# Performance work log

Measured on AMD Instinct MI355X. Metric: run time of the kernel, lower is better.

Reference implementation:

```python
import jax, jax.numpy as jnp
import numpy as np

B, CH, T, D = 16, 64, 2048, 1  # d must be 1 (tf.squeeze(x, axis=-1))
F = 8  # conv filters


def setup_inputs() -> dict:
    key = jax.random.key(0)
    k1, k2, k3, k4 = jax.random.split(key, 4)
    return {
        "x": jax.random.normal(k1, (B, CH, T, D), dtype=jnp.float32),
        "w1": jax.random.normal(k2, (D, F), dtype=jnp.float32) * 0.1,
        "b1": jnp.zeros((F,), dtype=jnp.float32),
        "w2": jax.random.normal(k3, (D, F), dtype=jnp.float32) * 0.1,
        "b2": jnp.zeros((F,), dtype=jnp.float32),
        "gamma": jax.random.normal(k4, (1,), dtype=jnp.float32) * 0.1,
    }


def reference(x, w1, b1, w2, b2, gamma):
    b, ch, t, d = x.shape
    # 1x1 Conv2D == per-position matmul over channel dim; then Permute((2,1,3)) + Reshape((t,-1))
    q = (jnp.matmul(x, w1) + b1)  # (b, ch, t, F)
    k = (jnp.matmul(x, w2) + b2)  # (b, ch, t, F)
    q = jnp.transpose(q, (0, 2, 1, 3)).reshape(b, t, ch * q.shape[-1])  # (b, t, ch*F)
    k = jnp.transpose(k, (0, 2, 1, 3)).reshape(b, t, ch * k.shape[-1])  # (b, t, ch*F)
    energy = jnp.einsum('btf,bsf->bts', q, k)  # (b, t, t)
    max_h = jnp.max(energy, axis=2, keepdims=True)
    min_h = jnp.min(energy, axis=2, keepdims=True)
    energy = (energy - min_h) / (max_h - min_h + 1e-8)
    attention = jax.nn.softmax(energy, axis=-1)  # (b, t, t)
    x_sq = x[..., 0]  # (b, ch, t)
    # matmul(x_sq, attention, transpose_b=True): out[b,c,i] = sum_j x_sq[b,c,j] * attention[b,i,j]
    mixed = jnp.einsum('bcj,bij->bci', x_sq, attention)  # (b, ch, t)
    return gamma[0] * mixed[..., None] + x  # (b, ch, t, 1)
```

## Files before the change

kernel.cpp:

```cpp
#include <hip/hip_runtime.h>
#include <hip/hip_bf16.h>

#define NB 16
#define NCH 64
#define NT 2048

typedef __attribute__((ext_vector_type(8)))  short bf8;
typedef __attribute__((ext_vector_type(4)))  short bf4;
typedef __attribute__((ext_vector_type(16))) float f16f;

#if defined(__has_builtin)
#if __has_builtin(__builtin_amdgcn_exp2f)
#define EXP2(x) __builtin_amdgcn_exp2f(x)
#else
#define EXP2(x) __expf((x) * 0.69314718056f)
#endif
#else
#define EXP2(x) __expf((x) * 0.69314718056f)
#endif

static __device__ __forceinline__ short f2b(float f) {
    unsigned u = __float_as_uint(f);
    u += 0x7fffu + ((u >> 16) & 1u);
    return (short)(u >> 16);
}

static __device__ __forceinline__ unsigned cvtpk(float lo, float hi) {
    unsigned r;
    asm("v_cvt_pk_bf16_f32 %0, %1, %2" : "=v"(r) : "v"(lo), "v"(hi));
    return r;
}
#define SWAP32(x, y) asm volatile("v_permlane32_swap_b32 %0, %1" : "+v"(x), "+v"(y))

__global__ __launch_bounds__(256)
void prep_k(const float* __restrict__ x, const float* __restrict__ b1p,
            const float* __restrict__ w2,
            float* __restrict__ Xw, short* __restrict__ xT, short* __restrict__ xn) {
    __shared__ float T[NCH][65];
    const int b = blockIdx.y, t0 = blockIdx.x * 64;
    const int tid = threadIdx.x;
    const float* xb = x + (size_t)b * NCH * NT;

    const int tt = (tid & 15) * 4;
    #pragma unroll
    for (int co = 0; co < 4; ++co) {
        int c = co * 16 + (tid >> 4);
        float4 v = *reinterpret_cast<const float4*>(&xb[(size_t)c * NT + t0 + tt]);
        T[c][tt] = v.x; T[c][tt + 1] = v.y; T[c][tt + 2] = v.z; T[c][tt + 3] = v.w;
        bf4 w; w[0] = f2b(v.x); w[1] = f2b(v.y); w[2] = f2b(v.z); w[3] = f2b(v.w);
        *reinterpret_cast<bf4*>(&xn[((size_t)b * NCH + c) * NT + t0 + tt]) = w;
    }
    __syncthreads();
    if (tid < 64) {
        float s2b1 = 0.f;
        #pragma unroll
        for (int f = 0; f < 8; ++f) s2b1 += b1p[f] * w2[f];
        float s = 0.f;
        #pragma unroll
        for (int c = 0; c < NCH; ++c) s += T[c][tid];
        Xw[b * NT + t0 + tid] = s2b1 * s;
    }
    const int row = tid >> 2, cs = (tid & 3) * 16;
    bf8 v0, v1;
    #pragma unroll
    for (int u = 0; u < 8; ++u) v0[u] = f2b(T[cs + u][row]);
    #pragma unroll
    for (int u = 0; u < 8; ++u) v1[u] = f2b(T[cs + 8 + u][row]);
    short* dst = xT + ((size_t)b * NT + t0 + row) * NCH + cs;
    *reinterpret_cast<bf8*>(dst) = v0;
    *reinterpret_cast<bf8*>(dst + 8) = v1;
}

__global__ __launch_bounds__(256)
void attn9_k(const float* __restrict__ w1, const float* __restrict__ w2,
             const float* __restrict__ gp,
             const float* __restrict__ Xw, const short* __restrict__ xT,
             const short* __restrict__ xn, const float* __restrict__ x,
             float* __restrict__ out) {
    __shared__ float mMn[4][32];
    __shared__ float mMx[4][32];
    __shared__ float mPS[4][32];
    __shared__ float mAcc[4][32][66];

    const int b  = blockIdx.y;
    const int i0 = blockIdx.x * 32;
    const int tid  = threadIdx.x;
    const int h    = tid >> 6;
    const int lane = tid & 63;
    const int il   = lane & 31;
    const int hi   = lane >> 5;
    const int hi8  = hi * 8;

    float s11 = 0.f;
    #pragma unroll
    for (int f = 0; f < 8; ++f) s11 += w1[f] * w2[f];
    const float g = gp[0];

    const short* xTb = xT + (size_t)b * NT * NCH;
    const short* xnb = xn + (size_t)b * NCH * NT;
    const float* xb  = x + (size_t)b * NCH * NT;
    const float* Xwb = Xw + b * NT;

    const short* brow = xTb + (size_t)(i0 + il) * NCH + hi8;
    const bf8 Bg0 = *reinterpret_cast<const bf8*>(brow);
    const bf8 Bg1 = *reinterpret_cast<const bf8*>(brow + 16);
    const bf8 Bg2 = *reinterpret_cast<const bf8*>(brow + 32);
    const bf8 Bg3 = *reinterpret_cast<const bf8*>(brow + 48);

    float rmn = 3.0e38f, rmx = -3.0e38f;

    for (int t = 0; t < 16; ++t) {
        const int jt = h * 512 + t * 32;
        const short* arow = xTb + (size_t)(jt + il) * NCH + hi8;
        bf8 a0 = *reinterpret_cast<const bf8*>(arow);
        bf8 a1 = *reinterpret_cast<const bf8*>(arow + 16);
        bf8 a2 = *reinterpret_cast<const bf8*>(arow + 32);
        bf8 a3 = *reinterpret_cast<const bf8*>(arow + 48);
        f16f acc = {0.f};
        acc = __builtin_amdgcn_mfma_f32_32x32x16_bf16(a0, Bg0, acc, 0, 0, 0);
        acc = __builtin_amdgcn_mfma_f32_32x32x16_bf16(a1, Bg1, acc, 0, 0, 0);
        acc = __builtin_amdgcn_mfma_f32_32x32x16_bf16(a2, Bg2, acc, 0, 0, 0);
        acc = __builtin_amdgcn_mfma_f32_32x32x16_bf16(a3, Bg3, acc, 0, 0, 0);
        const float4 tw0 = *reinterpret_cast<const float4*>(Xwb + jt + 4 * hi);
        const float4 tw1 = *reinterpret_cast<const float4*>(Xwb + jt + 8 + 4 * hi);
        const float4 tw2 = *reinterpret_cast<const float4*>(Xwb + jt + 16 + 4 * hi);
        const float4 tw3 = *reinterpret_cast<const float4*>(Xwb + jt + 24 + 4 * hi);
        const float tw[16] = { tw0.x, tw0.y, tw0.z, tw0.w, tw1.x, tw1.y, tw1.z, tw1.w,
                               tw2.x, tw2.y, tw2.z, tw2.w, tw3.x, tw3.y, tw3.z, tw3.w };
        #pragma unroll
        for (int r = 0; r < 16; ++r) {
            float e = fmaf(s11, acc[r], tw[r]);
            rmn = fminf(rmn, e);
            rmx = fmaxf(rmx, e);
        }
    }
    rmn = fminf(rmn, __shfl_xor(rmn, 32, 64));
    rmx = fmaxf(rmx, __shfl_xor(rmx, 32, 64));
    if (lane < 32) { mMn[h][lane] = rmn; mMx[h][lane] = rmx; }
    __syncthreads();

    float mn = mMn[0][il], mx = mMx[0][il];
    #pragma unroll
    for (int w = 1; w < 4; ++w) {
        mn = fminf(mn, mMn[w][il]);
        mx = fmaxf(mx, mMx[w][il]);
    }
    const float inv2 = 1.44269504f / (mx - mn + 1e-8f);
    const float A  = s11 * inv2;
    const float KI = -mn * inv2;

    f16f macc0 = {0.f}, macc1 = {0.f};
    float ps = 0.f;

    for (int t = 0; t < 16; ++t) {
        const int jt = h * 512 + t * 32;
        const short* arow = xTb + (size_t)(jt + il) * NCH + hi8;
        bf8 a0 = *reinterpret_cast<const bf8*>(arow);
        bf8 a1 = *reinterpret_cast<const bf8*>(arow + 16);
        bf8 a2 = *reinterpret_cast<const bf8*>(arow + 32);
        bf8 a3 = *reinterpret_cast<const bf8*>(arow + 48);
        f16f acc = {0.f};
        acc = __builtin_amdgcn_mfma_f32_32x32x16_bf16(a0, Bg0, acc, 0, 0, 0);
        acc = __builtin_amdgcn_mfma_f32_32x32x16_bf16(a1, Bg1, acc, 0, 0, 0);
        acc = __builtin_amdgcn_mfma_f32_32x32x16_bf16(a2, Bg2, acc, 0, 0, 0);
        acc = __builtin_amdgcn_mfma_f32_32x32x16_bf16(a3, Bg3, acc, 0, 0, 0);
        const float4 tw0 = *reinterpret_cast<const float4*>(Xwb + jt + 4 * hi);
        const float4 tw1 = *reinterpret_cast<const float4*>(Xwb + jt + 8 + 4 * hi);
        const float4 tw2 = *reinterpret_cast<const float4*>(Xwb + jt + 16 + 4 * hi);
        const float4 tw3 = *reinterpret_cast<const float4*>(Xwb + jt + 24 + 4 * hi);
        const float tw[16] = { tw0.x, tw0.y, tw0.z, tw0.w, tw1.x, tw1.y, tw1.z, tw1.w,
                               tw2.x, tw2.y, tw2.z, tw2.w, tw3.x, tw3.y, tw3.z, tw3.w };
        float p[16];
        #pragma unroll
        for (int r = 0; r < 16; ++r) {
            p[r] = EXP2(fmaf(A, acc[r], fmaf(tw[r], inv2, KI)));
            ps += p[r];
        }
        unsigned pk00 = cvtpk(p[0],  p[1]),  pk01 = cvtpk(p[2],  p[3]);
        unsigned pk10 = cvtpk(p[4],  p[5]),  pk11 = cvtpk(p[6],  p[7]);
        unsigned pk20 = cvtpk(p[8],  p[9]),  pk21 = cvtpk(p[10], p[11]);
        unsigned pk30 = cvtpk(p[12], p[13]), pk31 = cvtpk(p[14], p[15]);
        SWAP32(pk00, pk10); SWAP32(pk01, pk11);
        SWAP32(pk20, pk30); SWAP32(pk21, pk31);
        union { unsigned u[4]; bf8 v; } f0, f1;
        f0.u[0] = pk00; f0.u[1] = pk01; f0.u[2] = pk10; f0.u[3] = pk11;
        f1.u[0] = pk20; f1.u[1] = pk21; f1.u[2] = pk30; f1.u[3] = pk31;
        const short* xrow0 = xnb + (size_t)(il) * NT + jt + hi8;
        const short* xrow1 = xnb + (size_t)(32 + il) * NT + jt + hi8;
        bf8 m00 = *reinterpret_cast<const bf8*>(xrow0);
        bf8 m01 = *reinterpret_cast<const bf8*>(xrow0 + 16);
        bf8 m10 = *reinterpret_cast<const bf8*>(xrow1);
        bf8 m11 = *reinterpret_cast<const bf8*>(xrow1 + 16);
        macc0 = __builtin_amdgcn_mfma_f32_32x32x16_bf16(m00, f0.v, macc0, 0, 0, 0);
        macc0 = __builtin_amdgcn_mfma_f32_32x32x16_bf16(m01, f1.v, macc0, 0, 0, 0);
        macc1 = __builtin_amdgcn_mfma_f32_32x32x16_bf16(m10, f0.v, macc1, 0, 0, 0);
        macc1 = __builtin_amdgcn_mfma_f32_32x32x16_bf16(m11, f1.v, macc1, 0, 0, 0);
    }

    ps += __shfl_xor(ps, 32, 64);
    if (lane < 32) mPS[h][lane] = ps;

    #pragma unroll
    for (int r = 0; r < 16; ++r) {
        const int c = (r & 3) + 8 * (r >> 2) + 4 * hi;
        mAcc[h][il][c]      = macc0[r];
        mAcc[h][il][c + 32] = macc1[r];
    }
    __syncthreads();

    const int i_l = tid & 31, grp = tid >> 5;
    const float rs = mPS[0][i_l] + mPS[1][i_l] + mPS[2][i_l] + mPS[3][i_l];
    const float sc = g / rs;
    const int i = i0 + i_l;
    #pragma unroll
    for (int u = 0; u < 8; ++u) {
        const int c = grp * 8 + u;
        const float tot = mAcc[0][i_l][c] + mAcc[1][i_l][c]
                        + mAcc[2][i_l][c] + mAcc[3][i_l][c];
        out[((size_t)b * NCH + c) * NT + i] = fmaf(sc, tot, xb[(size_t)c * NT + i]);
    }
}

extern "C" void kernel_launch(void* const* d_in, const int* in_sizes, int n_in,
                              void* d_out, int out_size, void* d_ws, size_t ws_size,
                              hipStream_t stream) {
    const float* x     = (const float*)d_in[0];
    const float* w1    = (const float*)d_in[1];
    const float* b1    = (const float*)d_in[2];
    const float* w2    = (const float*)d_in[3];
    const float* gamma = (const float*)d_in[5];
    float* out = (float*)d_out;

    char* p = (char*)d_ws;
    float* Xw = (float*)p;   p += (size_t)NB * NT * 4;
    short* xT = (short*)p;   p += (size_t)NB * NT * NCH * 2;
    short* xn = (short*)p;

    hipLaunchKernelGGL(prep_k, dim3(NT / 64, NB), dim3(256), 0, stream,
                       x, b1, w2, Xw, xT, xn);
    hipLaunchKernelGGL(attn9_k, dim3(NT / 32, NB), dim3(256), 0, stream,
                       w1, w2, gamma, Xw, xT, xn, x, out);
}
```

Baseline: 115.1 us.

## Split key range across eight waves and remap blocks to XCDs by batch

The attention kernel now uses 512 threads, with eight waves each covering 256 key positions instead of four waves covering 512, which halves each wave's serial loop. The grid is flattened and remapped so that blocks of the same batch land on the same XCD, aiming for better L2 reuse of xT and xn. The partial mixed accumulators are staged in LDS as bf16 to keep shared memory small despite doubling the waves. In exchange there is a larger cross-wave reduction and extra precision loss from rounding the partial sums to bf16.

```diff
diff --git a/kernel.cpp b/kernel.cpp
--- a/kernel.cpp
+++ b/kernel.cpp
@@ -24,7 +24,9 @@
     u += 0x7fffu + ((u >> 16) & 1u);
     return (short)(u >> 16);
 }
-
+static __device__ __forceinline__ float b2f(short s) {
+    return __uint_as_float(((unsigned)(unsigned short)s) << 16);
+}
 static __device__ __forceinline__ unsigned cvtpk(float lo, float hi) {
     unsigned r;
     asm("v_cvt_pk_bf16_f32 %0, %1, %2" : "=v"(r) : "v"(lo), "v"(hi));
@@ -71,19 +73,23 @@
     *reinterpret_cast<bf8*>(dst + 8) = v1;
 }
 
-__global__ __launch_bounds__(256)
-void attn9_k(const float* __restrict__ w1, const float* __restrict__ w2,
-             const float* __restrict__ gp,
-             const float* __restrict__ Xw, const short* __restrict__ xT,
-             const short* __restrict__ xn, const float* __restrict__ x,
-             float* __restrict__ out) {
-    __shared__ float mMn[4][32];
-    __shared__ float mMx[4][32];
-    __shared__ float mPS[4][32];
-    __shared__ float mAcc[4][32][66];
-
-    const int b  = blockIdx.y;
-    const int i0 = blockIdx.x * 32;
+__global__ __launch_bounds__(512)
+void attn10_k(const float* __restrict__ w1, const float* __restrict__ w2,
+              const float* __restrict__ gp,
+              const float* __restrict__ Xw, const short* __restrict__ xT,
+              const short* __restrict__ xn, const float* __restrict__ x,
+              float* __restrict__ out) {
+    __shared__ float mMn[8][32];
+    __shared__ float mMx[8][32];
+    __shared__ float mPS[8][32];
+    __shared__ short mAcc[8][32][66];
+
+    const int bid  = blockIdx.x;
+    const int xcd  = bid & 7;
+    const int slot = bid >> 3;
+    const int b    = (xcd << 1) | (slot & 1);
+    const int i0   = (slot >> 1) << 5;
+
     const int tid  = threadIdx.x;
     const int h    = tid >> 6;
     const int lane = tid & 63;
@@ -109,8 +115,8 @@
 
     float rmn = 3.0e38f, rmx = -3.0e38f;
 
-    for (int t = 0; t < 16; ++t) {
-        const int jt = h * 512 + t * 32;
+    for (int t = 0; t < 8; ++t) {
+        const int jt = h * 256 + t * 32;
         const short* arow = xTb + (size_t)(jt + il) * NCH + hi8;
         bf8 a0 = *reinterpret_cast<const bf8*>(arow);
         bf8 a1 = *reinterpret_cast<const bf8*>(arow + 16);
@@ -141,7 +147,7 @@
 
     float mn = mMn[0][il], mx = mMx[0][il];
     #pragma unroll
-    for (int w = 1; w < 4; ++w) {
+    for (int w = 1; w < 8; ++w) {
         mn = fminf(mn, mMn[w][il]);
         mx = fmaxf(mx, mMx[w][il]);
     }
@@ -152,8 +158,8 @@
     f16f macc0 = {0.f}, macc1 = {0.f};
     float ps = 0.f;
 
-    for (int t = 0; t < 16; ++t) {
-        const int jt = h * 512 + t * 32;
+    for (int t = 0; t < 8; ++t) {
+        const int jt = h * 256 + t * 32;
         const short* arow = xTb + (size_t)(jt + il) * NCH + hi8;
         bf8 a0 = *reinterpret_cast<const bf8*>(arow);
         bf8 a1 = *reinterpret_cast<const bf8*>(arow + 16);
@@ -201,22 +207,25 @@
     if (lane < 32) mPS[h][lane] = ps;
 
     #pragma unroll
-    for (int r = 0; r < 16; ++r) {
+    for (int r = 0; r < 16; r += 2) {
         const int c = (r & 3) + 8 * (r >> 2) + 4 * hi;
-        mAcc[h][il][c]      = macc0[r];
-        mAcc[h][il][c + 32] = macc1[r];
+        *reinterpret_cast<unsigned*>(&mAcc[h][il][c])      = cvtpk(macc0[r], macc0[r + 1]);
+        *reinterpret_cast<unsigned*>(&mAcc[h][il][c + 32]) = cvtpk(macc1[r], macc1[r + 1]);
     }
     __syncthreads();
 
     const int i_l = tid & 31, grp = tid >> 5;
-    const float rs = mPS[0][i_l] + mPS[1][i_l] + mPS[2][i_l] + mPS[3][i_l];
+    float rs = 0.f;
+    #pragma unroll
+    for (int w = 0; w < 8; ++w) rs += mPS[w][i_l];
     const float sc = g / rs;
     const int i = i0 + i_l;
     #pragma unroll
-    for (int u = 0; u < 8; ++u) {
-        const int c = grp * 8 + u;
-        const float tot = mAcc[0][i_l][c] + mAcc[1][i_l][c]
-                        + mAcc[2][i_l][c] + mAcc[3][i_l][c];
+    for (int u = 0; u < 4; ++u) {
+        const int c = grp * 4 + u;
+        float tot = 0.f;
+        #pragma unroll
+        for (int w = 0; w < 8; ++w) tot += b2f(mAcc[w][i_l][c]);
         out[((size_t)b * NCH + c) * NT + i] = fmaf(sc, tot, xb[(size_t)c * NT + i]);
     }
 }
@@ -238,6 +247,6 @@
 
     hipLaunchKernelGGL(prep_k, dim3(NT / 64, NB), dim3(256), 0, stream,
                        x, b1, w2, Xw, xT, xn);
-    hipLaunchKernelGGL(attn9_k, dim3(NT / 32, NB), dim3(256), 0, stream,
+    hipLaunchKernelGGL(attn10_k, dim3(NB * NT / 32), dim3(512), 0, stream,
                        w1, w2, gamma, Xw, xT, xn, x, out);
 }
```

Result: no change. 115.9 us (+0.7%).
